# Performance work log

Hardware: AMD Instinct MI355X
Metric: run time of the kernel (lower is better)

Reference implementation:

```python
import jax, jax.numpy as jnp
import numpy as np

K_CHUNK = 512  # key-chunk size used by the module when n > 5000


def setup_inputs() -> dict:
    key = jax.random.key(0)
    ks = jax.random.split(key, 9)
    b, n, d = 1, 8192, 512
    s = 1.0 / np.sqrt(d)
    x = jax.random.normal(ks[0], (b, n, d), dtype=jnp.float32)
    Wq = jax.random.normal(ks[1], (d, d), dtype=jnp.float32) * s
    bq = jax.random.normal(ks[2], (d,), dtype=jnp.float32) * 0.01
    Wk = jax.random.normal(ks[3], (d, d), dtype=jnp.float32) * s
    bk = jax.random.normal(ks[4], (d,), dtype=jnp.float32) * 0.01
    Wv = jax.random.normal(ks[5], (d, d), dtype=jnp.float32) * s
    bv = jax.random.normal(ks[6], (d,), dtype=jnp.float32) * 0.01
    Wo = jax.random.normal(ks[7], (d, d), dtype=jnp.float32) * s
    bo = jax.random.normal(ks[8], (d,), dtype=jnp.float32) * 0.01
    return {"x": x, "Wq": Wq, "bq": bq, "Wk": Wk, "bk": bk,
            "Wv": Wv, "bv": bv, "Wo": Wo, "bo": bo}


def reference(x, Wq, bq, Wk, bk, Wv, bv, Wo, bo):
    # Faithful to the n > 5000 branch of SimpleAttenLayer (eval mode: dropout = identity).
    # The q-chunking in the original does not change the math (each q row is independent),
    # so we vectorize over all queries. The k-chunking DOES change the math: softmax is
    # applied within each 512-wide key block, then a second softmax over the concatenated
    # per-block weights, then matmul with full v.
    b, n, d = x.shape
    assert n % K_CHUNK == 0
    q = x @ Wq + bq
    k = x @ Wk + bk
    v = x @ Wv + bv
    scores = jnp.einsum('bnd,bmd->bnm', q, k) / jnp.sqrt(jnp.float32(d))
    # softmax within each key chunk of size K_CHUNK
    w1 = jax.nn.softmax(scores.reshape(b, n, n // K_CHUNK, K_CHUNK), axis=-1)
    w1 = w1.reshape(b, n, n)
    # second (global) softmax over the concatenated chunk weights
    w2 = jax.nn.softmax(w1, axis=-1)
    attn_out = jnp.einsum('bnm,bmd->bnd', w2, v)
    cls_attn_weights = w2[:, 0:1, :]  # [b, 1, n]
    out = x + (attn_out @ Wo + bo)
    return (out, cls_attn_weights)
```

## Files before the change

### kernel.cpp

```cpp
#include <hip/hip_runtime.h>
#include <stdint.h>

typedef unsigned short u16;
typedef uint8_t u8;
typedef __bf16 bf16x8 __attribute__((ext_vector_type(8)));
typedef float f32x4 __attribute__((ext_vector_type(4)));
typedef long i64x2 __attribute__((ext_vector_type(2)));

#define NTOK 8192
#define DD 512
#define CHK 512
#define NCH 16
#define KSPLIT 4
#define KLEN 2048
#define LOG2E 1.4426950408889634f
#define SCL 0.044194173824159216f
#define SCLL 0.063762069130835270f

__device__ __forceinline__ u16 f2bf(float f) {
  union { float f; uint32_t u; } v; v.f = f;
  uint32_t r = v.u + 0x7FFFu + ((v.u >> 16) & 1u);
  return (u16)(r >> 16);
}

template <int CTRL>
__device__ __forceinline__ float dppadd(float x) {
  int y = __builtin_amdgcn_update_dpp(0, __float_as_int(x), CTRL, 0xF, 0xF, true);
  return x + __int_as_float(y);
}
__device__ __forceinline__ float rowsum16(float x) {
  x = dppadd<0xB1>(x);
  x = dppadd<0x4E>(x);
  x = dppadd<0x141>(x);
  x = dppadd<0x140>(x);
  return x;
}

typedef const __attribute__((address_space(1))) unsigned int* gas_t;
typedef __attribute__((address_space(3))) unsigned int* las_t;
__device__ __forceinline__ void gload16(const void* g, void* l) {
  __builtin_amdgcn_global_load_lds((gas_t)g, (las_t)l, 16, 0, 0);
}

__device__ __forceinline__ void vm4bar() {
  asm volatile("s_waitcnt vmcnt(4)\n\ts_barrier" ::: "memory");
}
__device__ __forceinline__ void vm0bar() {
  asm volatile("s_waitcnt vmcnt(0)\n\ts_barrier" ::: "memory");
}
__device__ __forceinline__ void barx() {
  asm volatile("s_barrier" ::: "memory");
}
__device__ __forceinline__ void lgkm0() {
  asm volatile("s_waitcnt lgkmcnt(0)" ::: "memory");
  __builtin_amdgcn_sched_barrier(0);
}

__device__ __forceinline__ int ilv64(int p) {
  const int g = p >> 3;
  return (((g & 3) * 2) + (g >> 2)) * 8 + (p & 7);
}

__global__ void prep_kernel(const float* __restrict__ x, const float* __restrict__ Wq,
                            const float* __restrict__ Wk, const float* __restrict__ Wv,
                            const float* __restrict__ Wo, const float* __restrict__ bq,
                            u16* __restrict__ xb, u16* __restrict__ Wall, u16* __restrict__ WoT,
                            float* __restrict__ lsum, float* __restrict__ q0g) {
  __shared__ float t[32][33];
  const int bid = blockIdx.x;
  const int tid = threadIdx.x;
  if (bid < 4096) {
    int i = bid * 256 + tid;
    if (bid < 32) lsum[bid * 256 + tid] = 0.f;
    float4 v = ((const float4*)x)[i];
    ushort4 o;
    o.x = f2bf(v.x); o.y = f2bf(v.y); o.z = f2bf(v.z); o.w = f2bf(v.w);
    ((ushort4*)xb)[i] = o;
  } else if (bid < 5120) {
    const int tt = bid - 4096;
    const int z = tt >> 8, idx = tt & 255;
    const float* W; u16* WT;
    if (z == 0)      { W = Wq; WT = Wall; }
    else if (z == 1) { W = Wk; WT = Wall + 512 * 512; }
    else if (z == 2) { W = Wv; WT = Wall + 2 * 512 * 512; }
    else             { W = Wo; WT = WoT; }
    const int n0 = (idx & 15) * 32, k0 = (idx >> 4) * 32;
    const int tx = tid & 31, ty = tid >> 5;
    #pragma unroll
    for (int i = 0; i < 4; i++)
      t[ty + 8 * i][tx] = W[(k0 + ty + 8 * i) * DD + n0 + tx];
    __syncthreads();
    #pragma unroll
    for (int i = 0; i < 4; i++)
      WT[(n0 + ty + 8 * i) * DD + k0 + tx] = f2bf(t[tx][ty + 8 * i]);
  } else {
    const int c = (bid - 5120) * 256 + tid;
    float acc = bq[c];
    #pragma unroll 8
    for (int i = 0; i < 512; i++) acc += x[i] * Wq[i * 512 + c];
    q0g[c] = acc;
  }
}

__launch_bounds__(256, 3)
__global__ void qkv_kernel(const u16* __restrict__ A, const u16* __restrict__ Wall,
                           const float* __restrict__ bq, const float* __restrict__ bk,
                           const float* __restrict__ bv, u8* __restrict__ qb8,
                           u8* __restrict__ kb8, u8* __restrict__ vT8) {
  __shared__ __align__(16) u16 As[2][128 * 32];
  __shared__ __align__(16) u16 Bs[2][128 * 32];
  const int m0 = blockIdx.x * 128;
  const int n0g = blockIdx.y * 128;
  const int which = blockIdx.y >> 2;
  const int n0 = n0g & 511;
  const int tid = threadIdx.x;
  const int w = tid >> 6, lane = tid & 63, lm = lane & 15, quad = lane >> 4;
  const int wm = w & 1, wn = w >> 1;
  f32x4 acc[4][4] = {};
  const int soff = tid * 16;
  const int srow = soff >> 6;
  const int scol = soff & 63;
  const char* Ag = (const char*)A + ((size_t)(m0 + srow) * DD) * 2 + scol;
  const char* Bg = (const char*)Wall + ((size_t)(n0g + srow) * DD) * 2 + scol;
  char* Al = (char*)As + w * 1024;
  char* Bl = (char*)Bs + w * 1024;
  const size_t rs = (size_t)64 * DD * 2;

  auto stage = [&](int kk, int buf) {
    const char* ag = Ag + (size_t)kk * 2;
    const char* bg = Bg + (size_t)kk * 2;
    char* al = Al + buf * 8192;
    char* bl = Bl + buf * 8192;
    gload16(ag, al);
    gload16(ag + rs, al + 4096);
    gload16(bg, bl);
    gload16(bg + rs, bl + 4096);
  };

  stage(0, 0);
  for (int t = 0; t < 16; ++t) {
    const int cur = t & 1;
    if (t < 15) { stage((t + 1) * 32, cur ^ 1); vm4bar(); }
    else vm0bar();
    bf16x8 af[4], bfr[4];
    #pragma unroll
    for (int i = 0; i < 4; i++) af[i] = *(const bf16x8*)&As[cur][(wm * 64 + i * 16 + lm) * 32 + quad * 8];
    #pragma unroll
    for (int j = 0; j < 4; j++) bfr[j] = *(const bf16x8*)&Bs[cur][(wn * 64 + j * 16 + lm) * 32 + quad * 8];
    lgkm0();
    #pragma unroll
    for (int i = 0; i < 4; i++)
      #pragma unroll
      for (int j = 0; j < 4; j++)
        acc[i][j] = __builtin_amdgcn_mfma_f32_16x16x32_bf16(af[i], bfr[j], acc[i][j], 0, 0, 0);
    barx();
  }
  const float* bias = (which == 0) ? bq : (which == 1) ? bk : bv;
  u8* tile = (u8*)As;
  #pragma unroll
  for (int i = 0; i < 4; i++) {
    const int rl0 = wm * 64 + i * 16 + quad * 4;
    #pragma unroll
    for (int j = 0; j < 4; j++) {
      const int cl = wn * 64 + j * 16 + lm;
      const float bv_ = bias[n0 + cl];
      if (which == 2) {
        #pragma unroll
        for (int r = 0; r < 4; r++) {
          const float val = acc[i][j][r] + bv_;
          uint32_t pk = __builtin_amdgcn_cvt_pk_fp8_f32(val, val, 0, false);
          const int rl = rl0 + r;
          const int tl = (rl & 64) | ilv64(((rl & 15) << 2) | ((rl >> 4) & 3));
          tile[cl * 128 + tl] = (u8)(pk & 0xFF);
        }
      } else {
        const int icl = (cl & 64) | ilv64(cl & 63);
        #pragma unroll
        for (int r = 0; r < 4; r++) {
          const float val = acc[i][j][r] + bv_;
          uint32_t pk = __builtin_amdgcn_cvt_pk_fp8_f32(val, val, 0, false);
          tile[(rl0 + r) * 128 + icl] = (u8)(pk & 0xFF);
        }
      }
    }
  }
  __syncthreads();
  const int lrow = tid >> 1, half = tid & 1;
  const uint4* s4 = (const uint4*)(tile + lrow * 128 + half * 64);
  if (which == 2) {
    uint4* p = (uint4*)(vT8 + (size_t)(n0 + lrow) * NTOK + m0 + half * 64);
    #pragma unroll
    for (int k = 0; k < 4; k++) p[k] = s4[k];
  } else {
    u8* dst = (which == 0) ? qb8 : kb8;
    uint4* p = (uint4*)(dst + (size_t)(m0 + lrow) * DD + n0 + half * 64);
    #pragma unroll
    for (int k = 0; k < 4; k++) p[k] = s4[k];
  }
}

__launch_bounds__(256, 3)
__global__ void outproj_kernel(const u16* __restrict__ A, const u16* __restrict__ BT,
                               const float* __restrict__ bias, float* __restrict__ outp,
                               const float* __restrict__ resid) {
  __shared__ __align__(16) u16 As[2][128 * 32];
  __shared__ __align__(16) u16 Bs[2][128 * 32];
  const int m0 = blockIdx.x * 128, n0 = blockIdx.y * 128;
  const int tid = threadIdx.x;
  const int w = tid >> 6, lane = tid & 63, lm = lane & 15, quad = lane >> 4;
  const int wm = w & 1, wn = w >> 1;
  f32x4 acc[4][4] = {};
  const int soff = tid * 16;
  const int srow = soff >> 6;
  const int scol = soff & 63;
  const char* Ag = (const char*)A + ((size_t)(m0 + srow) * DD) * 2 + scol;
  const char* Bg = (const char*)BT + ((size_t)(n0 + srow) * DD) * 2 + scol;
  char* Al = (char*)As + w * 1024;
  char* Bl = (char*)Bs + w * 1024;
  const size_t rs = (size_t)64 * DD * 2;

  auto stage = [&](int kk, int buf) {
    const char* ag = Ag + (size_t)kk * 2;
    const char* bg = Bg + (size_t)kk * 2;
    char* al = Al + buf * 8192;
    char* bl = Bl + buf * 8192;
    gload16(ag, al);
    gload16(ag + rs, al + 4096);
    gload16(bg, bl);
    gload16(bg + rs, bl + 4096);
  };

  stage(0, 0);
  for (int t = 0; t < 16; ++t) {
    const int cur = t & 1;
    if (t < 15) { stage((t + 1) * 32, cur ^ 1); vm4bar(); }
    else vm0bar();
    bf16x8 af[4], bfr[4];
    #pragma unroll
    for (int i = 0; i < 4; i++) af[i] = *(const bf16x8*)&As[cur][(wm * 64 + i * 16 + lm) * 32 + quad * 8];
    #pragma unroll
    for (int j = 0; j < 4; j++) bfr[j] = *(const bf16x8*)&Bs[cur][(wn * 64 + j * 16 + lm) * 32 + quad * 8];
    lgkm0();
    #pragma unroll
    for (int i = 0; i < 4; i++)
      #pragma unroll
      for (int j = 0; j < 4; j++)
        acc[i][j] = __builtin_amdgcn_mfma_f32_16x16x32_bf16(af[i], bfr[j], acc[i][j], 0, 0, 0);
    barx();
  }
  #pragma unroll
  for (int i = 0; i < 4; i++) {
    const int row0 = m0 + wm * 64 + i * 16 + quad * 4;
    #pragma unroll
    for (int j = 0; j < 4; j++) {
      const int col = n0 + wn * 64 + j * 16 + lm;
      const float bv = bias[col];
      #pragma unroll
      for (int r = 0; r < 4; r++) {
        const size_t idx = (size_t)(row0 + r) * DD + col;
        outp[idx] = acc[i][j][r] + bv + resid[idx];
      }
    }
  }
}

template <int MODE>
__launch_bounds__(256, 3)
__global__ void gemm_fp8_kernel(const u8* __restrict__ A, const u8* __restrict__ BT,
                                int K, int lda, int ldb, void* __restrict__ outp,
                                const float* __restrict__ lsum) {
  __shared__ __align__(16) u8 As[2][128 * 64];
  __shared__ __align__(16) u8 Bs[2][128 * 64];
  const int m0 = blockIdx.x * 128, n0 = blockIdx.y * 128;
  const int tid = threadIdx.x;
  const int w = tid >> 6, lane = tid & 63, lm = lane & 15, quad = lane >> 4;
  const int wm = w & 1, wn = w >> 1;
  f32x4 acc[4][4] = {};
  const int srow = tid >> 2;
  const int scol = ((tid & 3) ^ ((srow >> 1) & 3)) * 16;
  const size_t kbase = (MODE == 4) ? (size_t)blockIdx.z * (size_t)K : 0;
  const u8* Ag = A + (size_t)(m0 + srow) * lda + kbase + scol;
  const u8* Bg = BT + (size_t)(n0 + srow) * ldb + kbase + scol;
  u8* Al = (u8*)As + w * 1024;
  u8* Bl = (u8*)Bs + w * 1024;
  const size_t ars = (size_t)64 * lda;
  const size_t brs = (size_t)64 * ldb;
  const int csel = ((quad ^ ((lm >> 1) & 3)) * 16);

  auto stage = [&](int kk, int buf) {
    const u8* ag = Ag + kk;
    const u8* bg = Bg + kk;
    u8* al = Al + buf * 8192;
    u8* bl = Bl + buf * 8192;
    gload16(ag, al);
    gload16(ag + ars, al + 4096);
    gload16(bg, bl);
    gload16(bg + brs, bl + 4096);
  };

  stage(0, 0);
  int cur = 0;
  for (int kk = 0; kk < K; kk += 64) {
    if (kk + 64 < K) { stage(kk + 64, cur ^ 1); vm4bar(); }
    else vm0bar();
    i64x2 afv[4], bfv[4];
    #pragma unroll
    for (int i = 0; i < 4; i++)
      afv[i] = *(const i64x2*)&As[cur][(wm * 64 + i * 16 + lm) * 64 + csel];
    #pragma unroll
    for (int j = 0; j < 4; j++)
      bfv[j] = *(const i64x2*)&Bs[cur][(wn * 64 + j * 16 + lm) * 64 + csel];
    lgkm0();
    #pragma unroll
    for (int i = 0; i < 4; i++)
      #pragma unroll
      for (int j = 0; j < 4; j++) {
        acc[i][j] = __builtin_amdgcn_mfma_f32_16x16x32_fp8_fp8(afv[i].x, bfv[j].x, acc[i][j], 0, 0, 0);
        acc[i][j] = __builtin_amdgcn_mfma_f32_16x16x32_fp8_fp8(afv[i].y, bfv[j].y, acc[i][j], 0, 0, 0);
      }
    barx();
    cur ^= 1;
  }
  #pragma unroll
  for (int i = 0; i < 4; i++) {
    const int row0 = m0 + wm * 64 + i * 16 + quad * 4;
    float li[4];
    if (MODE == 3) {
      #pragma unroll
      for (int r = 0; r < 4; r++) li[r] = 1.0f / lsum[row0 + r];
    }
    #pragma unroll
    for (int j = 0; j < 4; j++) {
      const int col = n0 + wn * 64 + j * 16 + lm;
      if (MODE == 3) {
        #pragma unroll
        for (int r = 0; r < 4; r++)
          ((u16*)outp)[(size_t)(row0 + r) * DD + col] = f2bf(acc[i][j][r] * li[r]);
      } else {
        float* po = (float*)outp + (size_t)blockIdx.z * NTOK * DD;
        #pragma unroll
        for (int r = 0; r < 4; r++)
          po[(size_t)(row0 + r) * DD + col] = acc[i][j][r];
      }
    }
  }
}

__global__ void pv_reduce_kernel(const float* __restrict__ part, const float* __restrict__ lsum,
                                 u16* __restrict__ attnb) {
  const int idx = blockIdx.x * 256 + threadIdx.x;
  const int row = idx >> 7;
  const int c4 = (idx & 127) << 2;
  const float* p = part + (size_t)row * DD + c4;
  const size_t stride = (size_t)NTOK * DD;
  float4 a = *(const float4*)(p);
  float4 b = *(const float4*)(p + stride);
  float4 c = *(const float4*)(p + 2 * stride);
  float4 d = *(const float4*)(p + 3 * stride);
  const float inv = 1.0f / lsum[row];
  ushort4 o;
  o.x = f2bf((a.x + b.x + c.x + d.x) * inv);
  o.y = f2bf((a.y + b.y + c.y + d.y) * inv);
  o.z = f2bf((a.z + b.z + c.z + d.z) * inv);
  o.w = f2bf((a.w + b.w + c.w + d.w) * inv);
  *(ushort4*)(attnb + (size_t)row * DD + c4) = o;
}

__launch_bounds__(512, 4)
__global__ void scores_kernel(const u8* __restrict__ qb8, const u8* __restrict__ kb8,
                              u8* __restrict__ P8, float* __restrict__ lsum) {
  __shared__ __align__(16) u8 As[2][64 * 64];
  __shared__ __align__(16) u8 Bs[2][512 * 64];
  __shared__ float hS[8][64], hP[8][64], hZ[64];
  const int m0 = blockIdx.x * 64;
  const int c = blockIdx.y;
  const int tid = threadIdx.x;
  const int w = tid >> 6, lane = tid & 63, lm = lane & 15, quad = lane >> 4;
  const int wsl = w;
  f32x4 s[4][4] = {};
  const int srA = tid >> 2;
  const int scS = ((tid & 3) ^ ((srA >> 1) & 3)) * 16;
  const u8* Qg = qb8 + (size_t)(m0 + srA) * DD + scS;
  const u8* Kg = kb8 + (size_t)(c * CHK + srA) * DD + scS;
  u8* Al = (u8*)As + w * 1024;
  u8* Bl = (u8*)Bs + w * 1024;
  const int csel = ((quad ^ ((lm >> 1) & 3)) * 16);

  auto stage = [&](int kk, int buf) {
    u8* al = Al + buf * 4096;
    u8* bl = Bl + buf * 32768;
    if (tid < 256) gload16(Qg + kk, al);
    gload16(Kg + kk, bl);
    gload16(Kg + kk + (size_t)128 * DD, bl + 8192);
    gload16(Kg + kk + (size_t)256 * DD, bl + 16384);
    gload16(Kg + kk + (size_t)384 * DD, bl + 24576);
  };

  stage(0, 0);
  vm0bar();
  #pragma unroll
  for (int t = 0; t < 8; ++t) {
    const int cur = t & 1;
    if (t < 7) stage((t + 1) * 64, cur ^ 1);
    i64x2 afv[4], bfv[4];
    #pragma unroll
    for (int i = 0; i < 4; i++)
      afv[i] = *(const i64x2*)&As[cur][(i * 16 + lm) * 64 + csel];
    #pragma unroll
    for (int j = 0; j < 4; j++)
      bfv[j] = *(const i64x2*)&Bs[cur][(wsl * 64 + j * 16 + lm) * 64 + csel];
    lgkm0();
    __builtin_amdgcn_s_setprio(1);
    #pragma unroll
    for (int i = 0; i < 4; i++)
      #pragma unroll
      for (int j = 0; j < 4; j++) {
        s[i][j] = __builtin_amdgcn_mfma_f32_16x16x32_fp8_fp8(afv[i].x, bfv[j].x, s[i][j], 0, 0, 0);
        s[i][j] = __builtin_amdgcn_mfma_f32_16x16x32_fp8_fp8(afv[i].y, bfv[j].y, s[i][j], 0, 0, 0);
      }
    __builtin_amdgcn_s_setprio(0);
    vm0bar();
  }
  #pragma unroll
  for (int i = 0; i < 4; i++) {
    #pragma unroll
    for (int reg = 0; reg < 4; reg++) {
      float z = 0.f;
      #pragma unroll
      for (int j = 0; j < 4; j++) {
        float e = exp2f(s[i][j][reg] * SCLL);
        s[i][j][reg] = e;
        z += e;
      }
      z = rowsum16(z);
      if (lm == 0) hS[wsl][i * 16 + quad * 4 + reg] = z;
    }
  }
  __syncthreads();
  if (tid < 64) {
    float t = 0.f;
    #pragma unroll
    for (int w2 = 0; w2 < 8; w2++) t += hS[w2][tid];
    hZ[tid] = LOG2E / t;
  }
  __syncthreads();
  const int newc = ((lm >> 1) & 3) * 2 + (lm >> 3);
  const int pbyte = wsl * 64 + newc * 8 + (lm & 1) * 4;
  #pragma unroll
  for (int i = 0; i < 4; i++) {
    #pragma unroll
    for (int reg = 0; reg < 4; reg++) {
      const int rl = i * 16 + quad * 4 + reg;
      const float iz = hZ[rl];
      const float p0 = exp2f(s[i][0][reg] * iz);
      const float p1 = exp2f(s[i][1][reg] * iz);
      const float p2 = exp2f(s[i][2][reg] * iz);
      const float p3 = exp2f(s[i][3][reg] * iz);
      float zp = (p0 + p1) + (p2 + p3);
      zp = rowsum16(zp);
      if (lm == 0) hP[wsl][rl] = zp;
      uint32_t o = __builtin_amdgcn_cvt_pk_fp8_f32(p0, p1, 0, false);
      o = __builtin_amdgcn_cvt_pk_fp8_f32(p2, p3, o, true);
      *(uint32_t*)(P8 + (size_t)(m0 + rl) * NTOK + c * CHK + pbyte) = o;
    }
  }
  __syncthreads();
  if (tid < 64) {
    float t = 0.f;
    #pragma unroll
    for (int w2 = 0; w2 < 8; w2++) t += hP[w2][tid];
    atomicAdd(&lsum[m0 + tid], t);
  }
}

__global__ void cls_u_kernel(const float* __restrict__ Wk, const float* __restrict__ bk,
                             const float* __restrict__ q0g, float* __restrict__ uc) {
  __shared__ float q0[512];
  const int tid = threadIdx.x;
  q0[tid] = q0g[tid];
  q0[tid + 256] = q0g[tid + 256];
  __syncthreads();
  if (blockIdx.x < 8) {
    const int c = blockIdx.x * 64 + (tid >> 2), ii = tid & 3;
    float acc = 0.f;
    #pragma unroll 8
    for (int j = ii; j < 512; j += 4) acc += Wk[(size_t)c * 512 + j] * q0[j];
    acc += __shfl_xor(acc, 1, 64);
    acc += __shfl_xor(acc, 2, 64);
    if (ii == 0) uc[c] = acc;
  } else if (tid < 64) {
    float acc = 0.f;
    #pragma unroll 8
    for (int j = tid; j < 512; j += 64) acc += bk[j] * q0[j];
    #pragma unroll
    for (int off = 1; off < 64; off <<= 1) acc += __shfl_xor(acc, off, 64);
    if (tid == 0) uc[512] = acc;
  }
}

__global__ void cls_scores_kernel(const float* __restrict__ x, const float* __restrict__ uc,
                                  float* __restrict__ s0) {
  __shared__ float u[512];
  __shared__ float c0s;
  int tid = threadIdx.x;
  for (int i = tid; i < 512; i += 256) u[i] = uc[i];
  if (tid == 0) c0s = uc[512];
  __syncthreads();
  int rowg = blockIdx.x * 32 + (tid >> 3);
  int ii = tid & 7;
  const float* xr = x + rowg * 512;
  float acc = 0.f;
  for (int i = ii; i < 512; i += 8) acc += xr[i] * u[i];
  acc += __shfl_xor(acc, 1, 64);
  acc += __shfl_xor(acc, 2, 64);
  acc += __shfl_xor(acc, 4, 64);
  if (ii == 0) s0[rowg] = (acc + c0s) * SCL;
}

__global__ void cls_softmax_kernel(const float* __restrict__ s0, float* __restrict__ out) {
  int tid = threadIdx.x;
  int w = tid >> 6, lane = tid & 63;
  const float* sc = s0 + w * 512;
  float v[8];
  float m = -1e30f;
  #pragma unroll
  for (int j = 0; j < 8; j++) { v[j] = sc[lane * 8 + j]; m = fmaxf(m, v[j]); }
  for (int off = 1; off < 64; off <<= 1) m = fmaxf(m, __shfl_xor(m, off, 64));
  float z = 0.f;
  #pragma unroll
  for (int j = 0; j < 8; j++) { v[j] = expf(v[j] - m); z += v[j]; }
  for (int off = 1; off < 64; off <<= 1) z += __shfl_xor(z, off, 64);
  float invz = 1.f / z;
  float l = 0.f;
  #pragma unroll
  for (int j = 0; j < 8; j++) { v[j] = expf(v[j] * invz); l += v[j]; }
  for (int off = 1; off < 64; off <<= 1) l += __shfl_xor(l, off, 64);
  __shared__ float lw[16];
  if (lane == 0) lw[w] = l;
  __syncthreads();
  float L = 0.f;
  for (int i = 0; i < 16; i++) L += lw[i];
  float invL = 1.f / L;
  #pragma unroll
  for (int j = 0; j < 8; j++) out[w * 512 + lane * 8 + j] = v[j] * invL;
}

extern "C" void kernel_launch(void* const* d_in, const int* in_sizes, int n_in,
                              void* d_out, int out_size, void* d_ws, size_t ws_size,
                              hipStream_t stream) {
  const float* x  = (const float*)d_in[0];
  const float* Wq = (const float*)d_in[1];
  const float* bq = (const float*)d_in[2];
  const float* Wk = (const float*)d_in[3];
  const float* bk = (const float*)d_in[4];
  const float* Wv = (const float*)d_in[5];
  const float* bv = (const float*)d_in[6];
  const float* Wo = (const float*)d_in[7];
  const float* bo = (const float*)d_in[8];
  float* out = (float*)d_out;

  char* ws = (char*)d_ws;
  u16* xb    = (u16*)(ws);
  u16* Wall  = (u16*)(ws + 8388608);
  u16* WoT   = (u16*)(ws + 9961472);
  u8*  qb8   = (u8*)(ws + 10485760);
  u8*  kb8   = (u8*)(ws + 14680064);
  u8*  vT8   = (u8*)(ws + 18874368);
  u16* attnb = (u16*)(ws + 23068672);
  float* q0g = (float*)(ws + 31457280);
  float* uc  = (float*)(ws + 31461376);
  float* s0  = (float*)(ws + 31465472);
  float* lsum= (float*)(ws + 31498240);
  u8*  P8    = (u8*)(ws + 31531008);
  float* part= (float*)(ws + 98639872);
  const size_t need_full = 98639872ULL + (size_t)KSPLIT * NTOK * DD * 4ULL;

  prep_kernel<<<5122, 256, 0, stream>>>(x, Wq, Wk, Wv, Wo, bq, xb, Wall, WoT, lsum, q0g);

  qkv_kernel<<<dim3(NTOK / 128, 12), 256, 0, stream>>>(xb, Wall, bq, bk, bv, qb8, kb8, vT8);

  scores_kernel<<<dim3(NTOK / 64, NCH), 512, 0, stream>>>(qb8, kb8, P8, lsum);

  if (ws_size >= need_full) {
    gemm_fp8_kernel<4><<<dim3(NTOK / 128, DD / 128, KSPLIT), 256, 0, stream>>>(
        P8, vT8, KLEN, NTOK, NTOK, part, nullptr);
    pv_reduce_kernel<<<NTOK * DD / 4 / 256, 256, 0, stream>>>(part, lsum, attnb);
  } else {
    gemm_fp8_kernel<3><<<dim3(NTOK / 128, DD / 128), 256, 0, stream>>>(
        P8, vT8, NTOK, NTOK, NTOK, attnb, lsum);
  }

  outproj_kernel<<<dim3(NTOK / 128, DD / 128), 256, 0, stream>>>(attnb, WoT, bo, out, x);

  cls_u_kernel<<<9, 256, 0, stream>>>(Wk, bk, q0g, uc);
  cls_scores_kernel<<<NTOK / 32, 256, 0, stream>>>(x, uc, s0);
  cls_softmax_kernel<<<1, 1024, 0, stream>>>(s0, out + (size_t)NTOK * DD);
}
```

Before: 299.3 us.

## Use 32x32x64 scaled FP8 MFMA for PV GEMM and halve K-split

Result: no change. 300.4 us (+0.4%).

```diff
diff --git a/kernel.cpp b/kernel.cpp
--- a/kernel.cpp
+++ b/kernel.cpp
@@ -5,14 +5,16 @@
 typedef uint8_t u8;
 typedef __bf16 bf16x8 __attribute__((ext_vector_type(8)));
 typedef float f32x4 __attribute__((ext_vector_type(4)));
+typedef float f32x16 __attribute__((ext_vector_type(16)));
 typedef long i64x2 __attribute__((ext_vector_type(2)));
+typedef int i32x8 __attribute__((ext_vector_type(8)));
 
 #define NTOK 8192
 #define DD 512
 #define CHK 512
 #define NCH 16
-#define KSPLIT 4
-#define KLEN 2048
+#define KSPLIT 2
+#define KLEN 4096
 #define LOG2E 1.4426950408889634f
 #define SCL 0.044194173824159216f
 #define SCLL 0.063762069130835270f
@@ -170,7 +172,8 @@
           const float val = acc[i][j][r] + bv_;
           uint32_t pk = __builtin_amdgcn_cvt_pk_fp8_f32(val, val, 0, false);
           const int rl = rl0 + r;
-          const int tl = (rl & 64) | ilv64(((rl & 15) << 2) | ((rl >> 4) & 3));
+          const int t6 = rl & 63;
+          const int tl = (rl & 64) | ((t6 & 15) * 4 + (t6 >> 4));
           tile[cl * 128 + tl] = (u8)(pk & 0xFF);
         }
       } else {
@@ -266,36 +269,34 @@
 
 template <int MODE>
 __launch_bounds__(256, 3)
-__global__ void gemm_fp8_kernel(const u8* __restrict__ A, const u8* __restrict__ BT,
-                                int K, int lda, int ldb, void* __restrict__ outp,
-                                const float* __restrict__ lsum) {
+__global__ void gemm_pv_kernel(const u8* __restrict__ A, const u8* __restrict__ BT,
+                               int K, void* __restrict__ outp,
+                               const float* __restrict__ lsum) {
   __shared__ __align__(16) u8 As[2][128 * 64];
   __shared__ __align__(16) u8 Bs[2][128 * 64];
   const int m0 = blockIdx.x * 128, n0 = blockIdx.y * 128;
   const int tid = threadIdx.x;
-  const int w = tid >> 6, lane = tid & 63, lm = lane & 15, quad = lane >> 4;
+  const int w = tid >> 6, lane = tid & 63;
+  const int l31 = lane & 31, kh = lane >> 5;
   const int wm = w & 1, wn = w >> 1;
-  f32x4 acc[4][4] = {};
+  f32x16 acc[2][2] = {};
   const int srow = tid >> 2;
   const int scol = ((tid & 3) ^ ((srow >> 1) & 3)) * 16;
-  const size_t kbase = (MODE == 4) ? (size_t)blockIdx.z * (size_t)K : 0;
-  const u8* Ag = A + (size_t)(m0 + srow) * lda + kbase + scol;
-  const u8* Bg = BT + (size_t)(n0 + srow) * ldb + kbase + scol;
+  const size_t kbase = (size_t)blockIdx.z * (size_t)K;
+  const u8* Ag = A + (size_t)(m0 + srow) * NTOK + kbase + scol;
+  const u8* Bg = BT + (size_t)(n0 + srow) * NTOK + kbase + scol;
   u8* Al = (u8*)As + w * 1024;
   u8* Bl = (u8*)Bs + w * 1024;
-  const size_t ars = (size_t)64 * lda;
-  const size_t brs = (size_t)64 * ldb;
-  const int csel = ((quad ^ ((lm >> 1) & 3)) * 16);
+  const size_t rs = (size_t)64 * NTOK;
+  const int s_ = (l31 >> 1) & 3;
+  const int c0 = ((kh * 2) ^ s_) * 16;
+  const int c1 = ((kh * 2 + 1) ^ s_) * 16;
 
   auto stage = [&](int kk, int buf) {
-    const u8* ag = Ag + kk;
-    const u8* bg = Bg + kk;
-    u8* al = Al + buf * 8192;
-    u8* bl = Bl + buf * 8192;
-    gload16(ag, al);
-    gload16(ag + ars, al + 4096);
-    gload16(bg, bl);
-    gload16(bg + brs, bl + 4096);
+    gload16(Ag + kk, Al + buf * 8192);
+    gload16(Ag + kk + rs, Al + buf * 8192 + 4096);
+    gload16(Bg + kk, Bl + buf * 8192);
+    gload16(Bg + kk + rs, Bl + buf * 8192 + 4096);
   };
 
   stage(0, 0);
@@ -303,44 +304,44 @@
   for (int kk = 0; kk < K; kk += 64) {
     if (kk + 64 < K) { stage(kk + 64, cur ^ 1); vm4bar(); }
     else vm0bar();
-    i64x2 afv[4], bfv[4];
-    #pragma unroll
-    for (int i = 0; i < 4; i++)
-      afv[i] = *(const i64x2*)&As[cur][(wm * 64 + i * 16 + lm) * 64 + csel];
-    #pragma unroll
-    for (int j = 0; j < 4; j++)
-      bfv[j] = *(const i64x2*)&Bs[cur][(wn * 64 + j * 16 + lm) * 64 + csel];
+    i32x8 av[2], bv[2];
+    #pragma unroll
+    for (int g = 0; g < 2; g++) {
+      const int ar = wm * 64 + g * 32 + l31;
+      union { i32x8 v; struct { i64x2 lo; i64x2 hi; } p; } ua;
+      ua.p.lo = *(const i64x2*)&As[cur][ar * 64 + c0];
+      ua.p.hi = *(const i64x2*)&As[cur][ar * 64 + c1];
+      av[g] = ua.v;
+      const int br = wn * 64 + g * 32 + l31;
+      union { i32x8 v; struct { i64x2 lo; i64x2 hi; } p; } ub;
+      ub.p.lo = *(const i64x2*)&Bs[cur][br * 64 + c0];
+      ub.p.hi = *(const i64x2*)&Bs[cur][br * 64 + c1];
+      bv[g] = ub.v;
+    }
     lgkm0();
     #pragma unroll
-    for (int i = 0; i < 4; i++)
-      #pragma unroll
-      for (int j = 0; j < 4; j++) {
-        acc[i][j] = __builtin_amdgcn_mfma_f32_16x16x32_fp8_fp8(afv[i].x, bfv[j].x, acc[i][j], 0, 0, 0);
-        acc[i][j] = __builtin_amdgcn_mfma_f32_16x16x32_fp8_fp8(afv[i].y, bfv[j].y, acc[i][j], 0, 0, 0);
-      }
+    for (int i = 0; i < 2; i++)
+      #pragma unroll
+      for (int j = 0; j < 2; j++)
+        acc[i][j] = __builtin_amdgcn_mfma_scale_f32_32x32x64_f8f6f4(
+            av[i], bv[j], acc[i][j], 0, 0, 0, 0x7F7F7F7F, 0, 0x7F7F7F7F);
     barx();
     cur ^= 1;
   }
   #pragma unroll
-  for (int i = 0; i < 4; i++) {
-    const int row0 = m0 + wm * 64 + i * 16 + quad * 4;
-    float li[4];
-    if (MODE == 3) {
-      #pragma unroll
-      for (int r = 0; r < 4; r++) li[r] = 1.0f / lsum[row0 + r];
-    }
-    #pragma unroll
-    for (int j = 0; j < 4; j++) {
-      const int col = n0 + wn * 64 + j * 16 + lm;
-      if (MODE == 3) {
-        #pragma unroll
-        for (int r = 0; r < 4; r++)
-          ((u16*)outp)[(size_t)(row0 + r) * DD + col] = f2bf(acc[i][j][r] * li[r]);
-      } else {
-        float* po = (float*)outp + (size_t)blockIdx.z * NTOK * DD;
-        #pragma unroll
-        for (int r = 0; r < 4; r++)
-          po[(size_t)(row0 + r) * DD + col] = acc[i][j][r];
+  for (int i = 0; i < 2; i++) {
+    #pragma unroll
+    for (int j = 0; j < 2; j++) {
+      #pragma unroll
+      for (int r = 0; r < 16; r++) {
+        const int row = m0 + wm * 64 + i * 32 + (r & 3) + 8 * (r >> 2) + 4 * kh;
+        const int col = n0 + wn * 64 + j * 32 + l31;
+        if (MODE == 3) {
+          ((u16*)outp)[(size_t)row * DD + col] = f2bf(acc[i][j][r] * (1.0f / lsum[row]));
+        } else {
+          float* po = (float*)outp + (size_t)blockIdx.z * NTOK * DD;
+          po[(size_t)row * DD + col] = acc[i][j][r];
+        }
       }
     }
   }
@@ -355,14 +356,12 @@
   const size_t stride = (size_t)NTOK * DD;
   float4 a = *(const float4*)(p);
   float4 b = *(const float4*)(p + stride);
-  float4 c = *(const float4*)(p + 2 * stride);
-  float4 d = *(const float4*)(p + 3 * stride);
   const float inv = 1.0f / lsum[row];
   ushort4 o;
-  o.x = f2bf((a.x + b.x + c.x + d.x) * inv);
-  o.y = f2bf((a.y + b.y + c.y + d.y) * inv);
-  o.z = f2bf((a.z + b.z + c.z + d.z) * inv);
-  o.w = f2bf((a.w + b.w + c.w + d.w) * inv);
+  o.x = f2bf((a.x + b.x) * inv);
+  o.y = f2bf((a.y + b.y) * inv);
+  o.z = f2bf((a.z + b.z) * inv);
+  o.w = f2bf((a.w + b.w) * inv);
   *(ushort4*)(attnb + (size_t)row * DD + c4) = o;
 }
 
@@ -444,8 +443,7 @@
     hZ[tid] = LOG2E / t;
   }
   __syncthreads();
-  const int newc = ((lm >> 1) & 3) * 2 + (lm >> 3);
-  const int pbyte = wsl * 64 + newc * 8 + (lm & 1) * 4;
+  const int pbyte = wsl * 64 + lm * 4;
   #pragma unroll
   for (int i = 0; i < 4; i++) {
     #pragma unroll
@@ -582,12 +580,12 @@
   scores_kernel<<<dim3(NTOK / 64, NCH), 512, 0, stream>>>(qb8, kb8, P8, lsum);
 
   if (ws_size >= need_full) {
-    gemm_fp8_kernel<4><<<dim3(NTOK / 128, DD / 128, KSPLIT), 256, 0, stream>>>(
-        P8, vT8, KLEN, NTOK, NTOK, part, nullptr);
+    gemm_pv_kernel<4><<<dim3(NTOK / 128, DD / 128, KSPLIT), 256, 0, stream>>>(
+        P8, vT8, KLEN, part, nullptr);
     pv_reduce_kernel<<<NTOK * DD / 4 / 256, 256, 0, stream>>>(part, lsum, attnb);
   } else {
-    gemm_fp8_kernel<3><<<dim3(NTOK / 128, DD / 128), 256, 0, stream>>>(
-        P8, vT8, NTOK, NTOK, NTOK, attnb, lsum);
+    gemm_pv_kernel<3><<<dim3(NTOK / 128, DD / 128), 256, 0, stream>>>(
+        P8, vT8, NTOK, attnb, lsum);
   }
 
   outproj_kernel<<<dim3(NTOK / 128, DD / 128), 256, 0, stream>>>(attnb, WoT, bo, out, x);
```
